# Performance work log

Measured on AMD Instinct MI355X. Metric: run time of the kernel, lower is better.

## Reference

```python
import jax, jax.numpy as jnp
import numpy as np

B, D, H, W = 32, 64, 64, 64
K = 1024

def setup_inputs() -> dict:
    key = jax.random.key(0)
    k1, k2 = jax.random.split(key)
    x = jax.random.normal(k1, (B, D, H, W), dtype=jnp.float32)
    # nn.Parameter(torch.rand(embeddings_dim, num_embeddings)) -> uniform [0,1)
    emb = jax.random.uniform(k2, (D, K), dtype=jnp.float32)
    return {"x": x, "emb": emb}


def reference(x, emb):
    # x: [B, D, H, W], emb: [D, K]
    b, d, h, w = x.shape
    xf = jnp.transpose(x, (0, 2, 3, 1)).reshape(-1, d)  # [N, D], N = B*H*W
    # squared L2 distance (same argmin as torch.norm(.,2) distance)
    d2 = (
        jnp.sum(xf * xf, axis=-1, keepdims=True)
        - 2.0 * (xf @ emb)
        + jnp.sum(emb * emb, axis=0)
    )  # [N, K]
    argmin = jnp.argmin(d2, axis=-1)  # [N]
    # gather codebook vectors: emb.T[argmin] -> [N, D]
    q = jnp.take(emb.T, argmin, axis=0)
    result = jnp.transpose(q.reshape(b, h, w, d), (0, 3, 1, 2))  # [B, D, H, W]
    return result, argmin.reshape(b, h, w)
```

## Files before the change

kernel.cpp:

```cpp
#include <hip/hip_runtime.h>


using half8 = __attribute__((ext_vector_type(8))) _Float16;
using half4 = __attribute__((ext_vector_type(4))) _Float16;
using f32x4 = __attribute__((ext_vector_type(4))) float;

#define XPITCH 72

__global__ void prep_kernel(const float* __restrict__ emb,
                            float* __restrict__ e2,
                            _Float16* __restrict__ eTh,
                            _Float16* __restrict__ eTl) {
    int k = blockIdx.x * 64 + threadIdx.x;
    float s = 0.f;
#pragma unroll
    for (int c = 0; c < 8; ++c) {
        half8 hv, lv;
#pragma unroll
        for (int j = 0; j < 8; ++j) {
            float v = emb[(c * 8 + j) * 1024 + k];
            s = fmaf(v, v, s);
            _Float16 h = (_Float16)v;
            hv[j] = h;
            lv[j] = (_Float16)(v - (float)h);
        }
        *(half8*)(eTh + k * 64 + c * 8) = hv;
        *(half8*)(eTl + k * 64 + c * 8) = lv;
    }
    e2[k] = s;
}

__launch_bounds__(256, 2)
__global__ void vq_kernel(const float* __restrict__ x,
                          const _Float16* __restrict__ eTh,
                          const _Float16* __restrict__ eTl,
                          const float* __restrict__ e2,
                          const float* __restrict__ emb,
                          float* __restrict__ outq,
                          float* __restrict__ outidx) {
    __shared__ _Float16 sxh[128 * XPITCH];
    __shared__ _Float16 sxl[128 * XPITCH];
    __shared__ float rbest[4 * 128];
    __shared__ int   ridx[4 * 128];
    __shared__ int   samin[128];

    const int tx = threadIdx.x;
    const int n0 = blockIdx.x * 128;
    const int bb = n0 >> 12;
    const int hw = n0 & 4095;
    const float* xbase = x + bb * 262144 + hw;

    {
        const int p     = tx & 127;
        const int dbase = (tx >> 7) << 5;
#pragma unroll
        for (int it = 0; it < 8; ++it) {
            int d0 = dbase + it * 4;
            float v0 = xbase[(d0 + 0) * 4096 + p];
            float v1 = xbase[(d0 + 1) * 4096 + p];
            float v2 = xbase[(d0 + 2) * 4096 + p];
            float v3 = xbase[(d0 + 3) * 4096 + p];
            _Float16 h0 = (_Float16)v0, h1 = (_Float16)v1,
                     h2 = (_Float16)v2, h3 = (_Float16)v3;
            half4 hv = {h0, h1, h2, h3};
            half4 lv = {(_Float16)(v0 - (float)h0), (_Float16)(v1 - (float)h1),
                        (_Float16)(v2 - (float)h2), (_Float16)(v3 - (float)h3)};
            *(half4*)(sxh + p * XPITCH + d0) = hv;
            *(half4*)(sxl + p * XPITCH + d0) = lv;
        }
    }
    __syncthreads();

    const int lane = tx & 63;
    const int w    = tx >> 6;
    const int r16  = lane & 15;
    const int q    = lane >> 4;

    half8 ah[8][2], al[8][2];
#pragma unroll
    for (int mt = 0; mt < 8; ++mt)
#pragma unroll
        for (int s = 0; s < 2; ++s) {
            ah[mt][s] = *(const half8*)(sxh + (mt * 16 + r16) * XPITCH + s * 32 + q * 8);
            al[mt][s] = *(const half8*)(sxl + (mt * 16 + r16) * XPITCH + s * 32 + q * 8);
        }
    asm volatile("" ::: "memory");

    float best[32];
    unsigned int bt[4] = {0u, 0u, 0u, 0u};
#pragma unroll
    for (int i = 0; i < 32; ++i) best[i] = 3.4e38f;

    const int kw = w << 8;
    const _Float16* bhbase = eTh + (kw + r16) * 64 + q * 8;
    const _Float16* blbase = eTl + (kw + r16) * 64 + q * 8;
    const float*    e2base = e2 + kw + r16;

    half8 pbh0, pbh1, pbl0, pbl1; float pe2;
    half8 qbh0, qbh1, qbl0, qbl1; float qe2;

#define LOADSET(BH0, BH1, BL0, BL1, E2V, TT)                                  \
    {                                                                         \
        const int off_ = (TT) << 10;                \
        BH0 = *(const half8*)(bhbase + off_);                                 \
        BH1 = *(const half8*)(bhbase + off_ + 32);                            \
        BL0 = *(const half8*)(blbase + off_);                                 \
        BL1 = *(const half8*)(blbase + off_ + 32);                            \
        E2V = e2base[(TT) << 4];                                              \
    }

#define COMPUTE(BH0, BH1, BL0, BL1, E2V, TT)                                  \
    {                                                                         \
        _Pragma("unroll")                                                     \
        for (int mt = 0; mt < 8; ++mt) {                                      \
            f32x4 a = {0.f, 0.f, 0.f, 0.f};                                   \
            a = __builtin_amdgcn_mfma_f32_16x16x32_f16(al[mt][0], BL0, a, 0, 0, 0); \
            a = __builtin_amdgcn_mfma_f32_16x16x32_f16(al[mt][1], BL1, a, 0, 0, 0); \
            a = __builtin_amdgcn_mfma_f32_16x16x32_f16(al[mt][0], BH0, a, 0, 0, 0); \
            a = __builtin_amdgcn_mfma_f32_16x16x32_f16(al[mt][1], BH1, a, 0, 0, 0); \
            a = __builtin_amdgcn_mfma_f32_16x16x32_f16(ah[mt][0], BL0, a, 0, 0, 0); \
            a = __builtin_amdgcn_mfma_f32_16x16x32_f16(ah[mt][1], BL1, a, 0, 0, 0); \
            a = __builtin_amdgcn_mfma_f32_16x16x32_f16(ah[mt][0], BH0, a, 0, 0, 0); \
            a = __builtin_amdgcn_mfma_f32_16x16x32_f16(ah[mt][1], BH1, a, 0, 0, 0); \
            _Pragma("unroll")                                                 \
            for (int rr = 0; rr < 4; ++rr) {                                  \
                float dist_ = fmaf(-2.f, a[rr], E2V);                         \
                const int i_ = mt * 4 + rr;                                   \
                const int sh_ = (i_ & 7) * 4;                                 \
                if (dist_ < best[i_]) {                                       \
                    best[i_] = dist_;                                         \
                    bt[i_ >> 3] = (bt[i_ >> 3] & ~(0xFu << sh_)) |            \
                                  ((unsigned int)(TT) << sh_);                \
                }                                                             \
            }                                                                 \
        }                                                                     \
    }

    LOADSET(pbh0, pbh1, pbl0, pbl1, pe2, 0);
#pragma unroll 1
    for (int t = 0; t < 16; t += 2) {
        LOADSET(qbh0, qbh1, qbl0, qbl1, qe2, t + 1);
        COMPUTE(pbh0, pbh1, pbl0, pbl1, pe2, t);
        LOADSET(pbh0, pbh1, pbl0, pbl1, pe2, (t + 2) & 15);
        COMPUTE(qbh0, qbh1, qbl0, qbl1, qe2, t + 1);
    }

#pragma unroll
    for (int mt = 0; mt < 8; ++mt)
#pragma unroll
        for (int rr = 0; rr < 4; ++rr) {
            const int i = mt * 4 + rr;
            float bv = best[i];
            int   bk = kw + (int)(((bt[i >> 3] >> ((i & 7) * 4)) & 15u) << 4) + r16;
#pragma unroll
            for (int m = 1; m < 16; m <<= 1) {
                float ov = __shfl_xor(bv, m, 64);
                int   ok = __shfl_xor(bk, m, 64);
                if (ov < bv || (ov == bv && ok < bk)) { bv = ov; bk = ok; }
            }
            if (r16 == 0) {
                const int p = mt * 16 + q * 4 + rr;
                rbest[w * 128 + p] = bv;
                ridx[w * 128 + p]  = bk;
            }
        }
    __syncthreads();

    if (tx < 128) {
        float bv = rbest[tx];
        int   bk = ridx[tx];
#pragma unroll
        for (int g = 1; g < 4; ++g) {
            float v  = rbest[g * 128 + tx];
            int   kk = ridx[g * 128 + tx];
            if (v < bv || (v == bv && kk < bk)) { bv = v; bk = kk; }
        }
        samin[tx] = bk;
        outidx[n0 + tx] = (float)bk;
    }
    __syncthreads();

    const int p = tx & 127;
    const int drow = tx >> 7;
    const int amin = samin[p];
    float* obase = outq + bb * 262144 + hw + p;
#pragma unroll
    for (int it = 0; it < 32; ++it) {
        int d = (it << 1) + drow;
        obase[d * 4096] = emb[d * 1024 + amin];
    }
}

extern "C" void kernel_launch(void* const* d_in, const int* in_sizes, int n_in,
                              void* d_out, int out_size, void* d_ws, size_t ws_size,
                              hipStream_t stream) {
    const float* x   = (const float*)d_in[0];
    const float* emb = (const float*)d_in[1];
    float* outq   = (float*)d_out;
    float* outidx = outq + 8388608;

    float*    e2  = (float*)d_ws;
    _Float16* eTh = (_Float16*)((char*)d_ws + 4096);
    _Float16* eTl = (_Float16*)((char*)d_ws + 4096 + 131072);

    prep_kernel<<<16, 64, 0, stream>>>(emb, e2, eTh, eTl);
    vq_kernel<<<1024, 256, 0, stream>>>(x, eTh, eTl, e2, emb, outq, outidx);
}
```

Measured before the change: 162.5 us.

## Split pixels across waves instead of codebook entries, removing cross-wave argmin reduction

```diff
diff --git a/kernel.cpp b/kernel.cpp
--- a/kernel.cpp
+++ b/kernel.cpp
@@ -30,7 +30,7 @@
     e2[k] = s;
 }
 
-__launch_bounds__(256, 2)
+__launch_bounds__(256, 4)
 __global__ void vq_kernel(const float* __restrict__ x,
                           const _Float16* __restrict__ eTh,
                           const _Float16* __restrict__ eTl,
@@ -40,9 +40,7 @@
                           float* __restrict__ outidx) {
     __shared__ _Float16 sxh[128 * XPITCH];
     __shared__ _Float16 sxl[128 * XPITCH];
-    __shared__ float rbest[4 * 128];
-    __shared__ int   ridx[4 * 128];
-    __shared__ int   samin[128];
+    __shared__ int samin[128];
 
     const int tx = threadIdx.x;
     const int n0 = blockIdx.x * 128;
@@ -75,26 +73,26 @@
     const int w    = tx >> 6;
     const int r16  = lane & 15;
     const int q    = lane >> 4;
+    const int pxb  = w << 5;
 
-    half8 ah[8][2], al[8][2];
+    half8 ah[2][2], al[2][2];
 #pragma unroll
-    for (int mt = 0; mt < 8; ++mt)
+    for (int mt = 0; mt < 2; ++mt)
 #pragma unroll
         for (int s = 0; s < 2; ++s) {
-            ah[mt][s] = *(const half8*)(sxh + (mt * 16 + r16) * XPITCH + s * 32 + q * 8);
-            al[mt][s] = *(const half8*)(sxl + (mt * 16 + r16) * XPITCH + s * 32 + q * 8);
+            ah[mt][s] = *(const half8*)(sxh + (pxb + mt * 16 + r16) * XPITCH + s * 32 + q * 8);
+            al[mt][s] = *(const half8*)(sxl + (pxb + mt * 16 + r16) * XPITCH + s * 32 + q * 8);
         }
     asm volatile("" ::: "memory");
 
-    float best[32];
-    unsigned int bt[4] = {0u, 0u, 0u, 0u};
+    float best[8];
+    int   bestt[8];
 #pragma unroll
-    for (int i = 0; i < 32; ++i) best[i] = 3.4e38f;
+    for (int i = 0; i < 8; ++i) { best[i] = 3.4e38f; bestt[i] = 0; }
 
-    const int kw = w << 8;
-    const _Float16* bhbase = eTh + (kw + r16) * 64 + q * 8;
-    const _Float16* blbase = eTl + (kw + r16) * 64 + q * 8;
-    const float*    e2base = e2 + kw + r16;
+    const _Float16* bhbase = eTh + r16 * 64 + q * 8;
+    const _Float16* blbase = eTl + r16 * 64 + q * 8;
+    const float*    e2base = e2 + r16;
 
     half8 pbh0, pbh1, pbl0, pbl1; float pe2;
     half8 qbh0, qbh1, qbl0, qbl1; float qe2;
@@ -112,7 +110,7 @@
 #define COMPUTE(BH0, BH1, BL0, BL1, E2V, TT)                                  \
     {                                                                         \
         _Pragma("unroll")                                                     \
-        for (int mt = 0; mt < 8; ++mt) {                                      \
+        for (int mt = 0; mt < 2; ++mt) {                                      \
             f32x4 a = {0.f, 0.f, 0.f, 0.f};                                   \
             a = __builtin_amdgcn_mfma_f32_16x16x32_f16(al[mt][0], BL0, a, 0, 0, 0); \
             a = __builtin_amdgcn_mfma_f32_16x16x32_f16(al[mt][1], BL1, a, 0, 0, 0); \
@@ -126,32 +124,27 @@
             for (int rr = 0; rr < 4; ++rr) {                                  \
                 float dist_ = fmaf(-2.f, a[rr], E2V);                         \
                 const int i_ = mt * 4 + rr;                                   \
-                const int sh_ = (i_ & 7) * 4;                                 \
-                if (dist_ < best[i_]) {                                       \
-                    best[i_] = dist_;                                         \
-                    bt[i_ >> 3] = (bt[i_ >> 3] & ~(0xFu << sh_)) |            \
-                                  ((unsigned int)(TT) << sh_);                \
-                }                                                             \
+                if (dist_ < best[i_]) { best[i_] = dist_; bestt[i_] = (TT); } \
             }                                                                 \
         }                                                                     \
     }
 
     LOADSET(pbh0, pbh1, pbl0, pbl1, pe2, 0);
 #pragma unroll 1
-    for (int t = 0; t < 16; t += 2) {
+    for (int t = 0; t < 64; t += 2) {
         LOADSET(qbh0, qbh1, qbl0, qbl1, qe2, t + 1);
         COMPUTE(pbh0, pbh1, pbl0, pbl1, pe2, t);
-        LOADSET(pbh0, pbh1, pbl0, pbl1, pe2, (t + 2) & 15);
+        LOADSET(pbh0, pbh1, pbl0, pbl1, pe2, (t + 2) & 63);
         COMPUTE(qbh0, qbh1, qbl0, qbl1, qe2, t + 1);
     }
 
 #pragma unroll
-    for (int mt = 0; mt < 8; ++mt)
+    for (int mt = 0; mt < 2; ++mt)
 #pragma unroll
         for (int rr = 0; rr < 4; ++rr) {
             const int i = mt * 4 + rr;
             float bv = best[i];
-            int   bk = kw + (int)(((bt[i >> 3] >> ((i & 7) * 4)) & 15u) << 4) + r16;
+            int   bk = (bestt[i] << 4) + r16;
 #pragma unroll
             for (int m = 1; m < 16; m <<= 1) {
                 float ov = __shfl_xor(bv, m, 64);
@@ -159,26 +152,13 @@
                 if (ov < bv || (ov == bv && ok < bk)) { bv = ov; bk = ok; }
             }
             if (r16 == 0) {
-                const int p = mt * 16 + q * 4 + rr;
-                rbest[w * 128 + p] = bv;
-                ridx[w * 128 + p]  = bk;
+                const int p = pxb + mt * 16 + q * 4 + rr;
+                samin[p] = bk;
             }
         }
     __syncthreads();
 
-    if (tx < 128) {
-        float bv = rbest[tx];
-        int   bk = ridx[tx];
-#pragma unroll
-        for (int g = 1; g < 4; ++g) {
-            float v  = rbest[g * 128 + tx];
-            int   kk = ridx[g * 128 + tx];
-            if (v < bv || (v == bv && kk < bk)) { bv = v; bk = kk; }
-        }
-        samin[tx] = bk;
-        outidx[n0 + tx] = (float)bk;
-    }
-    __syncthreads();
+    if (tx < 128) outidx[n0 + tx] = (float)samin[tx];
 
     const int p = tx & 127;
     const int drow = tx >> 7;
```

Result: slower. 210.2 us (+29.4%).
